# Kernel tuning notes

Hardware: AMD Instinct MI355X
Metric: run time of the kernel (lower is better)

Reference implementation:

```python
import jax, jax.numpy as jnp
import numpy as np

D_MODEL = 1024
N_HEADS = 16
D_K = D_MODEL // N_HEADS
D_FF = 4096
B, S = 2, 2048
EPS = 1e-5


def setup_inputs() -> dict:
    key = jax.random.key(0)
    ks = jax.random.split(key, 16)
    sc = 0.02
    inp = {
        'x': jax.random.normal(ks[0], (B, S, D_MODEL), dtype=jnp.float32),
        'mask': jnp.ones((B, 1, 1, S), dtype=jnp.int32),
        'Wq': jax.random.normal(ks[1], (D_MODEL, D_MODEL), dtype=jnp.float32) * sc,
        'bq': jnp.zeros((D_MODEL,), dtype=jnp.float32),
        'Wk': jax.random.normal(ks[2], (D_MODEL, D_MODEL), dtype=jnp.float32) * sc,
        'bk': jnp.zeros((D_MODEL,), dtype=jnp.float32),
        'Wv': jax.random.normal(ks[3], (D_MODEL, D_MODEL), dtype=jnp.float32) * sc,
        'bv': jnp.zeros((D_MODEL,), dtype=jnp.float32),
        'Wo': jax.random.normal(ks[4], (D_MODEL, D_MODEL), dtype=jnp.float32) * sc,
        'bo': jnp.zeros((D_MODEL,), dtype=jnp.float32),
        'W1': jax.random.normal(ks[5], (D_MODEL, D_FF), dtype=jnp.float32) * sc,
        'b1': jnp.zeros((D_FF,), dtype=jnp.float32),
        'W2': jax.random.normal(ks[6], (D_FF, D_MODEL), dtype=jnp.float32) * sc,
        'b2': jnp.zeros((D_MODEL,), dtype=jnp.float32),
        'g1': jnp.ones((D_MODEL,), dtype=jnp.float32),
        'be1': jnp.zeros((D_MODEL,), dtype=jnp.float32),
        'g2': jnp.ones((D_MODEL,), dtype=jnp.float32),
        'be2': jnp.zeros((D_MODEL,), dtype=jnp.float32),
    }
    return inp


def _layernorm(x, g, b):
    mu = jnp.mean(x, axis=-1, keepdims=True)
    var = jnp.mean(jnp.square(x - mu), axis=-1, keepdims=True)
    return (x - mu) * jax.lax.rsqrt(var + EPS) * g + b


def _split_heads(x):
    b, s, _ = x.shape
    return x.reshape(b, s, N_HEADS, D_K).transpose(0, 2, 1, 3)  # [B,H,S,Dk]


def reference(x, mask, Wq, bq, Wk, bk, Wv, bv, Wo, bo, W1, b1, W2, b2, g1, be1, g2, be2):
    Q = _split_heads(x @ Wq + bq)
    K = _split_heads(x @ Wk + bk)
    V = _split_heads(x @ Wv + bv)
    scores = jnp.einsum('bhqd,bhkd->bhqk', Q, K) / jnp.sqrt(jnp.float32(D_K))
    scores = jnp.where(mask == 0, -jnp.inf, scores)
    attn = jax.nn.softmax(scores, axis=-1)
    ctx = jnp.einsum('bhqk,bhkd->bhqd', attn, V)
    ctx = ctx.transpose(0, 2, 1, 3).reshape(x.shape[0], x.shape[1], D_MODEL)
    attn_out = ctx @ Wo + bo
    h = _layernorm(x + attn_out, g1, be1)
    ff = jax.nn.relu(h @ W1 + b1) @ W2 + b2
    return _layernorm(h + ff, g2, be2)
```

## Files before the change

### kernel.cpp

```cpp
#include <hip/hip_runtime.h>
#include <hip/hip_bf16.h>

#define D_MODELC 1024
#define D_FFC    4096
#define N_HEADSC 16
#define BATCHC   2
#define SEQC     2048
#define M_TOK    (BATCHC*SEQC)

typedef __attribute__((ext_vector_type(4)))  float f32x4;
typedef __attribute__((ext_vector_type(16))) float f32x16;
typedef __attribute__((ext_vector_type(8)))  short s16x8;
using bf16_t = __hip_bfloat16;

static __device__ __forceinline__ unsigned short f2bf_u16(float f) {
  bf16_t h = __float2bfloat16(f);
  return __builtin_bit_cast(unsigned short, h);
}

static __device__ __forceinline__ unsigned int cvt_pk_bf16(float lo, float hi2) {
  unsigned int r;
  asm("v_cvt_pk_bf16_f32 %0, %1, %2" : "=v"(r) : "v"(lo), "v"(hi2));
  return r;
}

#define PSWAP(a, b) asm volatile("v_permlane32_swap_b32 %0, %1" : "+v"(a), "+v"(b))

#define ASYNC_COPY16(dst_lds, src_g) \
  __builtin_amdgcn_global_load_lds((const __attribute__((address_space(1))) void*)(src_g), \
                                   (__attribute__((address_space(3))) void*)(dst_lds), 16, 0, 0)

__global__ __launch_bounds__(256) void k_prep(
    const float* __restrict__ x,
    const float* __restrict__ Wq, const float* __restrict__ Wk,
    const float* __restrict__ Wv, const float* __restrict__ Wo,
    const float* __restrict__ W1, const float* __restrict__ W2,
    const float* __restrict__ bq, const float* __restrict__ bk,
    const float* __restrict__ bv,
    bf16_t* __restrict__ x16, bf16_t* __restrict__ wqkvT, bf16_t* __restrict__ woT,
    bf16_t* __restrict__ w1T, bf16_t* __restrict__ w2T, float* __restrict__ bqkv) {
  __shared__ float tile[32][33];
  const int bidx = blockIdx.x;
  const int tid = threadIdx.x;

  if (bidx < 12288) {
    const float* in;
    bf16_t* out;
    int R, C, bx, by;
    if (bidx < 4096) {
      const int z = bidx >> 10, t = bidx & 1023;
      in = (z == 0) ? Wq : (z == 1) ? Wk : (z == 2) ? Wv : Wo;
      out = (z == 0) ? wqkvT : (z == 1) ? wqkvT + 1024 * 1024
           : (z == 2) ? wqkvT + 2 * 1024 * 1024 : woT;
      R = 1024; C = 1024; bx = t & 31; by = t >> 5;
    } else if (bidx < 8192) {
      const int t = bidx - 4096;
      in = W1; out = w1T; R = 1024; C = 4096; bx = t & 127; by = t >> 7;
    } else {
      const int t = bidx - 8192;
      in = W2; out = w2T; R = 4096; C = 1024; bx = t & 31; by = t >> 5;
    }
    const int tx = tid & 31, ty = tid >> 5;
    const int c0 = bx * 32, r0 = by * 32;
#pragma unroll
    for (int i = 0; i < 4; ++i)
      tile[ty + i * 8][tx] = in[(size_t)(r0 + ty + i * 8) * C + c0 + tx];
    __syncthreads();
#pragma unroll
    for (int i = 0; i < 4; ++i)
      out[(size_t)(c0 + ty + i * 8) * R + r0 + tx] = __float2bfloat16(tile[tx][ty + i * 8]);
  } else if (bidx < 16384) {
    const int i = (bidx - 12288) * 256 + tid;
    float4 v = ((const float4*)x)[i];
    short4 o;
    o.x = (short)f2bf_u16(v.x);
    o.y = (short)f2bf_u16(v.y);
    o.z = (short)f2bf_u16(v.z);
    o.w = (short)f2bf_u16(v.w);
    ((short4*)x16)[i] = o;
  } else {
    const int i = (bidx - 16384) * 256 + tid;
    float v = (i < 1024) ? bq[i] : (i < 2048) ? bk[i - 1024] : bv[i - 2048];
    bqkv[i] = v;
  }
}

#define GBK 64

__global__ __launch_bounds__(256, 2) void k_gemm(
    const bf16_t* __restrict__ A, const bf16_t* __restrict__ BT,
    const float* __restrict__ bias,
    float* __restrict__ p0, float* __restrict__ p1,
    void* __restrict__ Cout, int M, int N, int K,
    int lda, int ldb, int ldc, int mode, int nsplit) {
  __shared__ __align__(16) bf16_t Asm[128 * GBK];
  __shared__ __align__(16) bf16_t Bsm[128 * GBK];

  const int nbn = N / 128;
  const int nwg = gridDim.x;
  const int cpx = nwg >> 3;
  int wg = (blockIdx.x & 7) * cpx + (blockIdx.x >> 3);
  int kslice = 0;
  if (nsplit == 2) { kslice = wg & 1; wg >>= 1; }
  const int mb = wg / nbn, nb = wg % nbn;
  const int row0 = mb * 128, col0 = nb * 128;
  A  += (size_t)kslice * K;
  BT += (size_t)kslice * K;

  const int tid = threadIdx.x;
  const int w = tid >> 6, lane = tid & 63;
  const int lr = lane & 15, lg = lane >> 4;
  const int wr = w >> 1, wc = w & 1;
  const int wbase = tid & 192;

  f32x4 acc[4][4];
#pragma unroll
  for (int m = 0; m < 4; ++m)
#pragma unroll
    for (int n = 0; n < 4; ++n) acc[m][n] = (f32x4){0.f, 0.f, 0.f, 0.f};

  for (int k0 = 0; k0 < K; k0 += GBK) {
    __syncthreads();
#pragma unroll
    for (int i = 0; i < 4; ++i) {
      int c = i * 256 + tid;
      int row = c >> 3;
      int sg = (c & 7) ^ (row & 7);
      ASYNC_COPY16(Asm + (size_t)(i * 256 + wbase) * 8,
                   A + (size_t)(row0 + row) * lda + k0 + sg * 8);
    }
#pragma unroll
    for (int i = 0; i < 4; ++i) {
      int c = i * 256 + tid;
      int row = c >> 3;
      int sg = (c & 7) ^ (row & 7);
      ASYNC_COPY16(Bsm + (size_t)(i * 256 + wbase) * 8,
                   BT + (size_t)(col0 + row) * ldb + k0 + sg * 8);
    }
    __syncthreads();
#pragma unroll
    for (int kst = 0; kst < 2; ++kst) {
      const int sl = ((kst * 4 + lg) ^ (lr & 7)) * 8;
      s16x8 af[4], bfr[4];
#pragma unroll
      for (int m = 0; m < 4; ++m)
        af[m] = *(const s16x8*)(Asm + (size_t)(wr * 64 + m * 16 + lr) * GBK + sl);
#pragma unroll
      for (int n = 0; n < 4; ++n)
        bfr[n] = *(const s16x8*)(Bsm + (size_t)(wc * 64 + n * 16 + lr) * GBK + sl);
#pragma unroll
      for (int m = 0; m < 4; ++m)
#pragma unroll
        for (int n = 0; n < 4; ++n)
          acc[m][n] = __builtin_amdgcn_mfma_f32_16x16x32_bf16(af[m], bfr[n], acc[m][n], 0, 0, 0);
    }
  }

  float* outf = (kslice == 0) ? p0 : p1;
  bf16_t* outh = (bf16_t*)Cout;
#pragma unroll
  for (int m = 0; m < 4; ++m) {
    int grow = row0 + wr * 64 + m * 16 + lg * 4;
#pragma unroll
    for (int n = 0; n < 4; ++n) {
      int gcol = col0 + wc * 64 + n * 16 + lr;
      float bv = (mode == 4) ? 0.f : bias[gcol];
      float cs = (mode == 3 && gcol < 1024) ? 0.18033688f : 1.f;
#pragma unroll
      for (int r = 0; r < 4; ++r) {
        float v = (acc[m][n][r] + bv) * cs;
        size_t idx = (size_t)(grow + r) * ldc + gcol;
        if (mode == 4) {
          outf[idx] = v;
        } else {
          if (mode == 1) v = fmaxf(v, 0.f);
          outh[idx] = __float2bfloat16(v);
        }
      }
    }
  }
}

__global__ __launch_bounds__(256, 4) void k_attn(
    const bf16_t* __restrict__ qkv, const int* __restrict__ mask,
    float* __restrict__ pA, float* __restrict__ pB,
    float* __restrict__ psA, float* __restrict__ psB) {
  const int bid = blockIdx.x;
  const int half = bid >> 9;
  const int inner = bid & 511;
  const int qt = inner & 15;
  const int h  = (inner >> 4) & 15;
  const int b  = inner >> 8;
  const int tid = threadIdx.x;
  const int w = tid >> 6, lane = tid & 63;
  const int l31 = lane & 31, hi = lane >> 5;
  const int wbase = tid & 192;

  __shared__ __align__(16) bf16_t Kl[2][64][64];
  __shared__ __align__(16) bf16_t Vl[2][4096];
  __shared__ __align__(16) float  mskf[2][68];

  const int tokb = b * SEQC;
  const int q0 = qt * 128 + w * 32;
  const int kb0 = half * (SEQC / 2);

  s16x8 qfrag[4];
  {
    const bf16_t* qp = qkv + (size_t)(tokb + q0 + l31) * 3072 + h * 64 + hi * 8;
#pragma unroll
    for (int s = 0; s < 4; ++s) qfrag[s] = *(const s16x8*)(qp + s * 16);
  }

  char* klc = (char*)&Kl[0][0][0];
  bf16_t* Vl0 = &Vl[0][0];
  const unsigned vbase =
      (unsigned)(size_t)(__attribute__((address_space(3))) bf16_t*)Vl0 + lane * 8;

  int vkey0, vd0, vkey1, vd1;
  {
    int c = tid, L = c >> 3;
    int f_ = L >> 4, t_ = (L >> 3) & 1, db_ = (L >> 2) & 1, h_ = (L >> 1) & 1, dl_ = L & 1;
    vkey0 = 16 * f_ + 8 * h_ + 4 * t_ + ((c & 7) >> 1);
    vd0 = ((db_ * 2 + dl_) << 4) + (c & 1) * 8;
  }
  {
    int c = tid + 256, L = c >> 3;
    int f_ = L >> 4, t_ = (L >> 3) & 1, db_ = (L >> 2) & 1, h_ = (L >> 1) & 1, dl_ = L & 1;
    vkey1 = 16 * f_ + 8 * h_ + 4 * t_ + ((c & 7) >> 1);
    vd1 = ((db_ * 2 + dl_) << 4) + (c & 1) * 8;
  }
  const bf16_t* srcV0 = qkv + (size_t)(tokb + kb0 + vkey0) * 3072 + 2048 + (size_t)h * 64 + vd0;
  const bf16_t* srcV1 = qkv + (size_t)(tokb + kb0 + vkey1) * 3072 + 2048 + (size_t)h * 64 + vd1;

  float mreg = 1.f;

#define STAGE_K(buf, kb)                                                              \
  {                                                                                   \
    _Pragma("unroll")                                                                 \
    for (int ii = 0; ii < 2; ++ii) {                                                  \
      int chunk = w * 2 + ii;                                                         \
      int row = chunk * 8 + (lane >> 3);                                              \
      int seg = (lane & 7) ^ (row & 7);                                               \
      const bf16_t* src = qkv + (size_t)(tokb + (kb) + row) * 3072 + 1024 + h * 64 + seg * 8; \
      ASYNC_COPY16(&Kl[buf][chunk * 8][0], src);                                      \
    }                                                                                 \
  }

#define STAGE_V(buf)                                                                  \
  {                                                                                   \
    ASYNC_COPY16(Vl0 + (size_t)(buf) * 4096 + (size_t)wbase * 8, srcV0);              \
    ASYNC_COPY16(Vl0 + (size_t)(buf) * 4096 + (size_t)(256 + wbase) * 8, srcV1);      \
    srcV0 += 64 * 3072;                                                               \
    srcV1 += 64 * 3072;                                                               \
  }

#define STAGE_M(buf, kb)                                                              \
  {                                                                                   \
    if (w == 0) {                                                                     \
      mreg = mask[tokb + (kb) + lane] ? 1.f : 0.f;                                    \
      mskf[buf][lane] = mreg;                                                         \
      unsigned long long z = __ballot(mreg == 0.f);                                   \
      if (lane == 0) mskf[buf][64] = (z == 0ull) ? 1.f : 0.f;                         \
    }                                                                                 \
  }

  STAGE_K(0, kb0)
  STAGE_V(0)
  STAGE_M(0, kb0)

  f32x16 o[2];
#pragma unroll
  for (int d = 0; d < 2; ++d)
#pragma unroll
    for (int i = 0; i < 16; ++i) o[d][i] = 0.f;
  float psum = 0.f;

  __syncthreads();

  for (int kt = 0; kt < SEQC / 128; ++kt) {
    const int kb = kb0 + kt * 64;
    const int cur = kt & 1, nxt = cur ^ 1;
    const bool more = (kt < SEQC / 128 - 1);

    if (more) {
      STAGE_K(nxt, kb + 64)
      STAGE_V(nxt)
      STAGE_M(nxt, kb + 64)
    }

    f32x16 st[2];
#pragma unroll
    for (int kk = 0; kk < 2; ++kk)
#pragma unroll
      for (int i = 0; i < 16; ++i) st[kk][i] = 0.f;
#pragma unroll
    for (int step = 0; step < 4; ++step) {
#pragma unroll
      for (int kb2 = 0; kb2 < 2; ++kb2) {
        int key = kb2 * 32 + l31;
        int seg = (2 * step + hi) ^ (lane & 7);
        s16x8 kf = *(const s16x8*)(klc + cur * 8192 + key * 128 + seg * 16);
        st[kb2] = __builtin_amdgcn_mfma_f32_32x32x16_bf16(kf, qfrag[step], st[kb2], 0, 0, 0);
      }
    }

    const bool allv = (mskf[cur][64] != 0.f);
    s16x8 pf[4];
#pragma unroll
    for (int kb2 = 0; kb2 < 2; ++kb2) {
      float pa[16];
      if (allv) {
#pragma unroll
        for (int i = 0; i < 16; ++i) {
          float e = __builtin_exp2f(st[kb2][i]);
          pa[i] = e;
          psum += e;
        }
      } else {
#pragma unroll
        for (int g = 0; g < 4; ++g) {
          f32x4 mm = *(const f32x4*)((char*)&mskf[cur][0] + (kb2 * 128 + g * 32 + hi * 16));
#pragma unroll
          for (int rr = 0; rr < 4; ++rr) {
            float e = __builtin_exp2f(st[kb2][g * 4 + rr]) * mm[rr];
            pa[g * 4 + rr] = e;
            psum += e;
          }
        }
      }
      unsigned int wv[8];
#pragma unroll
      for (int u = 0; u < 8; ++u) wv[u] = cvt_pk_bf16(pa[2 * u], pa[2 * u + 1]);
      unsigned int a0 = wv[0], b0 = wv[2]; PSWAP(a0, b0);
      unsigned int a1 = wv[1], b1 = wv[3]; PSWAP(a1, b1);
      unsigned int a2 = wv[4], b2 = wv[6]; PSWAP(a2, b2);
      unsigned int a3 = wv[5], b3 = wv[7]; PSWAP(a3, b3);
      uint4 u0 = {a0, a1, b0, b1};
      uint4 u1 = {a2, a3, b2, b3};
      pf[kb2 * 2 + 0] = __builtin_bit_cast(s16x8, u0);
      pf[kb2 * 2 + 1] = __builtin_bit_cast(s16x8, u1);
    }

    const unsigned va = vbase + cur * 8192;
#pragma unroll
    for (int db = 0; db < 2; ++db) {
      ulong tr[4][2];
#pragma unroll
      for (int f = 0; f < 4; ++f)
        asm volatile("ds_read_b64_tr_b16 %0, %2 offset:%c3\n\t"
                     "ds_read_b64_tr_b16 %1, %2 offset:%c4"
                     : "=v"(tr[f][0]), "=v"(tr[f][1])
                     : "v"(va), "i"((f * 16 + db * 4) * 128), "i"((f * 16 + 8 + db * 4) * 128));
      asm volatile("s_waitcnt lgkmcnt(0)" ::: "memory");
      __builtin_amdgcn_sched_barrier(0);
#pragma unroll
      for (int f = 0; f < 4; ++f) {
        ulong2 uv = {tr[f][0], tr[f][1]};
        s16x8 vfr = __builtin_bit_cast(s16x8, uv);
        o[db] = __builtin_amdgcn_mfma_f32_32x32x16_bf16(pf[f], vfr, o[db], 0, 0, 0);
      }
    }

    __syncthreads();
  }

  psum += __shfl_xor(psum, 32);
  float* po = half ? pB : pA;
  float* ps = half ? psB : psA;
#pragma unroll
  for (int dblk = 0; dblk < 2; ++dblk)
#pragma unroll
    for (int r = 0; r < 16; ++r) {
      int qq = (r & 3) + 8 * (r >> 2) + 4 * hi;
      int tok = tokb + q0 + qq;
      po[(size_t)tok * 1024 + h * 64 + dblk * 32 + l31] = o[dblk][r];
    }
  if (hi == 0)
    ps[(size_t)(tokb + q0 + l31) * 16 + h] = psum;
#undef STAGE_K
#undef STAGE_V
#undef STAGE_M
}

__global__ __launch_bounds__(256) void k_attn_merge(
    const float* __restrict__ pA, const float* __restrict__ pB,
    const float* __restrict__ psA, const float* __restrict__ psB,
    bf16_t* __restrict__ ctx) {
  const int row = blockIdx.x, tid = threadIdx.x;
  const size_t base = (size_t)row * 1024;
  const float4 a = ((const float4*)(pA + base))[tid];
  const float4 b = ((const float4*)(pB + base))[tid];
  const int hh = tid >> 4;
  const float rs = psA[row * 16 + hh] + psB[row * 16 + hh];
  const float inv = 1.f / rs;
  short4 ob;
  ob.x = (short)f2bf_u16((a.x + b.x) * inv);
  ob.y = (short)f2bf_u16((a.y + b.y) * inv);
  ob.z = (short)f2bf_u16((a.z + b.z) * inv);
  ob.w = (short)f2bf_u16((a.w + b.w) * inv);
  ((short4*)(ctx + base))[tid] = ob;
}

__global__ __launch_bounds__(256) void k_ln_res2(
    const float* __restrict__ p0, const float* __restrict__ p1,
    const float* __restrict__ res, const float* __restrict__ bias,
    const float* __restrict__ g, const float* __restrict__ be,
    float* __restrict__ outf, bf16_t* __restrict__ outh) {
  const int row = blockIdx.x, tid = threadIdx.x;
  const size_t base = (size_t)row * D_MODELC;
  const float4 a  = ((const float4*)(p0 + base))[tid];
  const float4 bq = ((const float4*)(p1 + base))[tid];
  const float4 c  = ((const float4*)(res + base))[tid];
  const float4 bi = ((const float4*)bias)[tid];
  float4 v;
  v.x = a.x + bq.x + c.x + bi.x;
  v.y = a.y + bq.y + c.y + bi.y;
  v.z = a.z + bq.z + c.z + bi.z;
  v.w = a.w + bq.w + c.w + bi.w;
  float s1 = v.x + v.y + v.z + v.w;
  float s2 = v.x * v.x + v.y * v.y + v.z * v.z + v.w * v.w;
#pragma unroll
  for (int mm = 1; mm < 64; mm <<= 1) {
    s1 += __shfl_xor(s1, mm);
    s2 += __shfl_xor(s2, mm);
  }
  __shared__ float sa[4], sb[4];
  const int wv = tid >> 6;
  if ((tid & 63) == 0) { sa[wv] = s1; sb[wv] = s2; }
  __syncthreads();
  s1 = sa[0] + sa[1] + sa[2] + sa[3];
  s2 = sb[0] + sb[1] + sb[2] + sb[3];
  const float mu = s1 * (1.f / D_MODELC);
  const float var = s2 * (1.f / D_MODELC) - mu * mu;
  const float rsq = rsqrtf(var + 1e-5f);
  const float4 gg = ((const float4*)g)[tid];
  const float4 bb = ((const float4*)be)[tid];
  float4 oo;
  oo.x = (v.x - mu) * rsq * gg.x + bb.x;
  oo.y = (v.y - mu) * rsq * gg.y + bb.y;
  oo.z = (v.z - mu) * rsq * gg.z + bb.z;
  oo.w = (v.w - mu) * rsq * gg.w + bb.w;
  ((float4*)(outf + base))[tid] = oo;
  if (outh) {
    short4 ob;
    ob.x = (short)f2bf_u16(oo.x);
    ob.y = (short)f2bf_u16(oo.y);
    ob.z = (short)f2bf_u16(oo.z);
    ob.w = (short)f2bf_u16(oo.w);
    ((short4*)(outh + base))[tid] = ob;
  }
}

extern "C" void kernel_launch(void* const* d_in, const int* in_sizes, int n_in,
                              void* d_out, int out_size, void* d_ws, size_t ws_size,
                              hipStream_t stream) {
  (void)in_sizes; (void)n_in; (void)out_size; (void)ws_size;
  const float* x   = (const float*)d_in[0];
  const int* mask  = (const int*)d_in[1];
  const float* Wq  = (const float*)d_in[2];
  const float* bq  = (const float*)d_in[3];
  const float* Wk  = (const float*)d_in[4];
  const float* bk  = (const float*)d_in[5];
  const float* Wv  = (const float*)d_in[6];
  const float* bv  = (const float*)d_in[7];
  const float* Wo  = (const float*)d_in[8];
  const float* bo  = (const float*)d_in[9];
  const float* W1  = (const float*)d_in[10];
  const float* b1  = (const float*)d_in[11];
  const float* W2  = (const float*)d_in[12];
  const float* b2  = (const float*)d_in[13];
  const float* g1  = (const float*)d_in[14];
  const float* be1 = (const float*)d_in[15];
  const float* g2  = (const float*)d_in[16];
  const float* be2 = (const float*)d_in[17];

  char* ws = (char*)d_ws;
  const size_t D = D_MODELC, F = D_FFC, M = M_TOK;
  const size_t SZ_X16  = M * D * 2;
  const size_t SZ_QKV  = M * 3 * D * 2;
  bf16_t* x16   = (bf16_t*)ws;
  bf16_t* ff1   = (bf16_t*)ws;
  bf16_t* qkvb  = (bf16_t*)(ws + SZ_X16);
  size_t off = SZ_X16 + SZ_QKV;
  bf16_t* ctx   = (bf16_t*)(ws + off); off += M * D * 2;
  bf16_t* wqkvT = (bf16_t*)(ws + off); off += 3 * D * D * 2;
  bf16_t* woT   = (bf16_t*)(ws + off); off += D * D * 2;
  bf16_t* w1T   = (bf16_t*)(ws + off); off += D * F * 2;
  bf16_t* w2T   = (bf16_t*)(ws + off); off += D * F * 2;
  float*  partA = (float*)(ws + off);  off += M * D * 4;
  float*  hbuf  = (float*)(ws + off);  off += M * D * 4;
  bf16_t* h16   = (bf16_t*)(ws + off); off += M * D * 2;
  float*  partB = (float*)(ws + off);  off += M * D * 4;
  float*  bqkv  = (float*)(ws + off);  off += 3 * D * 4;
  float*  psA   = (float*)(ws + off);  off += M * 16 * 4;
  float*  psB   = (float*)(ws + off);  off += M * 16 * 4;

  k_prep<<<16396, 256, 0, stream>>>(x, Wq, Wk, Wv, Wo, W1, W2, bq, bk, bv,
                                    x16, wqkvT, woT, w1T, w2T, bqkv);

  k_gemm<<<768, 256, 0, stream>>>(x16, wqkvT, bqkv, nullptr, nullptr, qkvb,
                                  4096, 3072, 1024, 1024, 1024, 3072, 3, 1);

  k_attn<<<1024, 256, 0, stream>>>(qkvb, mask, partA, partB, psA, psB);
  k_attn_merge<<<4096, 256, 0, stream>>>(partA, partB, psA, psB, ctx);

  k_gemm<<<512, 256, 0, stream>>>(ctx, woT, nullptr, partA, partB, nullptr,
                                  4096, 1024, 512, 1024, 1024, 1024, 4, 2);
  k_ln_res2<<<4096, 256, 0, stream>>>(partA, partB, x, bo, g1, be1, hbuf, h16);

  k_gemm<<<1024, 256, 0, stream>>>(h16, w1T, b1, nullptr, nullptr, ff1,
                                   4096, 4096, 1024, 1024, 1024, 4096, 1, 1);
  k_gemm<<<512, 256, 0, stream>>>(ff1, w2T, nullptr, partA, partB, nullptr,
                                  4096, 1024, 2048, 4096, 4096, 1024, 4, 2);
  k_ln_res2<<<4096, 256, 0, stream>>>(partA, partB, hbuf, b2, g2, be2, (float*)d_out, nullptr);
}
```

Before: 252.2 us.

## Add 256x256 double-buffered GEMM kernel for QKV and FFN1 projections

Adds a 512-thread GEMM kernel with 256x256 output tiles, two LDS buffers with async copies prefetched two k-steps ahead, split half-K fragment loads, and s_setprio around the MFMA bursts. It replaces the 128x128 kernel for the QKV and FFN up-projections to raise operand reuse per tile and overlap loads with MFMA work. The attention kernel also switches K and mask staging to incrementally advanced pointers, removing per-iteration address math. The larger tile gives fewer workgroups (192 and 256) on a large-CU device, which can leave CUs idle, and uses 128 KB of LDS per block.

```diff
diff --git a/kernel.cpp b/kernel.cpp
--- a/kernel.cpp
+++ b/kernel.cpp
@@ -85,6 +85,120 @@
   }
 }
 
+__global__ __launch_bounds__(512, 2) void k_gemm256(
+    const bf16_t* __restrict__ A, const bf16_t* __restrict__ BT,
+    const float* __restrict__ bias, bf16_t* __restrict__ Cout,
+    int N, int K, int lda, int ldb, int ldc, int mode) {
+  __shared__ __align__(16) bf16_t Ab[2][256][64];
+  __shared__ __align__(16) bf16_t Bb[2][256][64];
+
+  const int nbn = N / 256;
+  const int nwg = gridDim.x;
+  const int cpx = nwg >> 3;
+  const int wg = (blockIdx.x & 7) * cpx + (blockIdx.x >> 3);
+  const int mb = wg / nbn, nb = wg % nbn;
+  const int row0 = mb * 256, col0 = nb * 256;
+
+  const int tid = threadIdx.x;
+  const int w = tid >> 6, lane = tid & 63;
+  const int lr = lane & 15, lg = lane >> 4;
+  const int wr = w >> 2, wc = w & 3;
+  const int s7 = lr & 7;
+
+#define STAGE256(buf, kt_)                                                            \
+  {                                                                                   \
+    const int k0_ = (kt_) * 64;                                                       \
+    _Pragma("unroll")                                                                 \
+    for (int i_ = 0; i_ < 4; ++i_) {                                                  \
+      int c_ = tid + i_ * 512;                                                        \
+      int row_ = c_ >> 3, sg_ = (c_ & 7) ^ (row_ & 7);                                \
+      ASYNC_COPY16(&Ab[buf][0][0] + (size_t)c_ * 8,                                   \
+                   A + (size_t)(row0 + row_) * lda + k0_ + sg_ * 8);                  \
+    }                                                                                 \
+    _Pragma("unroll")                                                                 \
+    for (int i_ = 0; i_ < 4; ++i_) {                                                  \
+      int c_ = tid + i_ * 512;                                                        \
+      int row_ = c_ >> 3, sg_ = (c_ & 7) ^ (row_ & 7);                                \
+      ASYNC_COPY16(&Bb[buf][0][0] + (size_t)c_ * 8,                                   \
+                   BT + (size_t)(col0 + row_) * ldb + k0_ + sg_ * 8);                 \
+    }                                                                                 \
+  }
+
+  f32x4 acc[8][4];
+#pragma unroll
+  for (int m = 0; m < 8; ++m)
+#pragma unroll
+    for (int n = 0; n < 4; ++n) acc[m][n] = (f32x4){0.f, 0.f, 0.f, 0.f};
+
+  const int nt = K / 64;
+  STAGE256(0, 0)
+  STAGE256(1, 1)
+  asm volatile("s_waitcnt vmcnt(8)" ::: "memory");
+  __builtin_amdgcn_sched_barrier(0);
+  __builtin_amdgcn_s_barrier();
+
+  for (int t = 0; t < nt; ++t) {
+    const int cur = t & 1;
+    s16x8 a0[8], b0[4];
+#pragma unroll
+    for (int m = 0; m < 8; ++m)
+      a0[m] = *(const s16x8*)(&Ab[cur][wr * 128 + m * 16 + lr][(lg ^ s7) * 8]);
+#pragma unroll
+    for (int n = 0; n < 4; ++n)
+      b0[n] = *(const s16x8*)(&Bb[cur][wc * 64 + n * 16 + lr][(lg ^ s7) * 8]);
+    __builtin_amdgcn_s_setprio(1);
+#pragma unroll
+    for (int m = 0; m < 8; ++m)
+#pragma unroll
+      for (int n = 0; n < 4; ++n)
+        acc[m][n] = __builtin_amdgcn_mfma_f32_16x16x32_bf16(a0[m], b0[n], acc[m][n], 0, 0, 0);
+    __builtin_amdgcn_s_setprio(0);
+    s16x8 a1[8], b1[4];
+#pragma unroll
+    for (int m = 0; m < 8; ++m)
+      a1[m] = *(const s16x8*)(&Ab[cur][wr * 128 + m * 16 + lr][((4 + lg) ^ s7) * 8]);
+#pragma unroll
+    for (int n = 0; n < 4; ++n)
+      b1[n] = *(const s16x8*)(&Bb[cur][wc * 64 + n * 16 + lr][((4 + lg) ^ s7) * 8]);
+    asm volatile("s_waitcnt lgkmcnt(0)" ::: "memory");
+    __builtin_amdgcn_sched_barrier(0);
+    __builtin_amdgcn_s_barrier();
+    if (t + 2 < nt) STAGE256(cur, t + 2)
+    __builtin_amdgcn_s_setprio(1);
+#pragma unroll
+    for (int m = 0; m < 8; ++m)
+#pragma unroll
+      for (int n = 0; n < 4; ++n)
+        acc[m][n] = __builtin_amdgcn_mfma_f32_16x16x32_bf16(a1[m], b1[n], acc[m][n], 0, 0, 0);
+    __builtin_amdgcn_s_setprio(0);
+    if (t + 2 < nt) {
+      asm volatile("s_waitcnt vmcnt(8)" ::: "memory");
+    } else {
+      asm volatile("s_waitcnt vmcnt(0)" ::: "memory");
+    }
+    __builtin_amdgcn_sched_barrier(0);
+    __builtin_amdgcn_s_barrier();
+  }
+
+#pragma unroll
+  for (int m = 0; m < 8; ++m) {
+    int grow = row0 + wr * 128 + m * 16 + lg * 4;
+#pragma unroll
+    for (int n = 0; n < 4; ++n) {
+      int gcol = col0 + wc * 64 + n * 16 + lr;
+      float bv = bias[gcol];
+      float cs = (mode == 3 && gcol < 1024) ? 0.18033688f : 1.f;
+#pragma unroll
+      for (int r = 0; r < 4; ++r) {
+        float v = (acc[m][n][r] + bv) * cs;
+        if (mode == 1) v = fmaxf(v, 0.f);
+        Cout[(size_t)(grow + r) * ldc + gcol] = __float2bfloat16(v);
+      }
+    }
+  }
+#undef STAGE256
+}
+
 #define GBK 64
 
 __global__ __launch_bounds__(256, 2) void k_gemm(
@@ -165,7 +279,7 @@
     for (int n = 0; n < 4; ++n) {
       int gcol = col0 + wc * 64 + n * 16 + lr;
       float bv = (mode == 4) ? 0.f : bias[gcol];
-      float cs = (mode == 3 && gcol < 1024) ? 0.18033688f : 1.f;
+      float cs = 1.f;
 #pragma unroll
       for (int r = 0; r < 4; ++r) {
         float v = (acc[m][n][r] + bv) * cs;
@@ -231,19 +345,22 @@
   }
   const bf16_t* srcV0 = qkv + (size_t)(tokb + kb0 + vkey0) * 3072 + 2048 + (size_t)h * 64 + vd0;
   const bf16_t* srcV1 = qkv + (size_t)(tokb + kb0 + vkey1) * 3072 + 2048 + (size_t)h * 64 + vd1;
+  const int krow0 = ((w * 2 + 0) * 8) + (lane >> 3);
+  const int krow1 = ((w * 2 + 1) * 8) + (lane >> 3);
+  const bf16_t* srcK0 = qkv + (size_t)(tokb + kb0 + krow0) * 3072 + 1024 + (size_t)h * 64
+                        + (((lane & 7) ^ (krow0 & 7)) * 8);
+  const bf16_t* srcK1 = qkv + (size_t)(tokb + kb0 + krow1) * 3072 + 1024 + (size_t)h * 64
+                        + (((lane & 7) ^ (krow1 & 7)) * 8);
+  const int* mptr = mask + tokb + kb0 + lane;
 
   float mreg = 1.f;
 
-#define STAGE_K(buf, kb)                                                              \
+#define STAGE_K(buf)                                                                  \
   {                                                                                   \
-    _Pragma("unroll")                                                                 \
-    for (int ii = 0; ii < 2; ++ii) {                                                  \
-      int chunk = w * 2 + ii;                                                         \
-      int row = chunk * 8 + (lane >> 3);                                              \
-      int seg = (lane & 7) ^ (row & 7);                                               \
-      const bf16_t* src = qkv + (size_t)(tokb + (kb) + row) * 3072 + 1024 + h * 64 + seg * 8; \
-      ASYNC_COPY16(&Kl[buf][chunk * 8][0], src);                                      \
-    }                                                                                 \
+    ASYNC_COPY16(&Kl[buf][(w * 2 + 0) * 8][0], srcK0);                                \
+    ASYNC_COPY16(&Kl[buf][(w * 2 + 1) * 8][0], srcK1);                                \
+    srcK0 += 64 * 3072;                                                               \
+    srcK1 += 64 * 3072;                                                               \
   }
 
 #define STAGE_V(buf)                                                                  \
@@ -254,19 +371,20 @@
     srcV1 += 64 * 3072;                                                               \
   }
 
-#define STAGE_M(buf, kb)                                                              \
+#define STAGE_M(buf)                                                                  \
   {                                                                                   \
     if (w == 0) {                                                                     \
-      mreg = mask[tokb + (kb) + lane] ? 1.f : 0.f;                                    \
+      mreg = *mptr ? 1.f : 0.f;                                                       \
       mskf[buf][lane] = mreg;                                                         \
       unsigned long long z = __ballot(mreg == 0.f);                                   \
       if (lane == 0) mskf[buf][64] = (z == 0ull) ? 1.f : 0.f;                         \
     }                                                                                 \
-  }
-
-  STAGE_K(0, kb0)
+    mptr += 64;                                                                       \
+  }
+
+  STAGE_K(0)
   STAGE_V(0)
-  STAGE_M(0, kb0)
+  STAGE_M(0)
 
   f32x16 o[2];
 #pragma unroll
@@ -278,14 +396,13 @@
   __syncthreads();
 
   for (int kt = 0; kt < SEQC / 128; ++kt) {
-    const int kb = kb0 + kt * 64;
     const int cur = kt & 1, nxt = cur ^ 1;
     const bool more = (kt < SEQC / 128 - 1);
 
     if (more) {
-      STAGE_K(nxt, kb + 64)
+      STAGE_K(nxt)
       STAGE_V(nxt)
-      STAGE_M(nxt, kb + 64)
+      STAGE_M(nxt)
     }
 
     f32x16 st[2];
@@ -498,8 +615,8 @@
   k_prep<<<16396, 256, 0, stream>>>(x, Wq, Wk, Wv, Wo, W1, W2, bq, bk, bv,
                                     x16, wqkvT, woT, w1T, w2T, bqkv);
 
-  k_gemm<<<768, 256, 0, stream>>>(x16, wqkvT, bqkv, nullptr, nullptr, qkvb,
-                                  4096, 3072, 1024, 1024, 1024, 3072, 3, 1);
+  k_gemm256<<<192, 512, 0, stream>>>(x16, wqkvT, bqkv, qkvb,
+                                     3072, 1024, 1024, 1024, 3072, 3);
 
   k_attn<<<1024, 256, 0, stream>>>(qkvb, mask, partA, partB, psA, psB);
   k_attn_merge<<<4096, 256, 0, stream>>>(partA, partB, psA, psB, ctx);
@@ -508,8 +625,8 @@
                                   4096, 1024, 512, 1024, 1024, 1024, 4, 2);
   k_ln_res2<<<4096, 256, 0, stream>>>(partA, partB, x, bo, g1, be1, hbuf, h16);
 
-  k_gemm<<<1024, 256, 0, stream>>>(h16, w1T, b1, nullptr, nullptr, ff1,
-                                   4096, 4096, 1024, 1024, 1024, 4096, 1, 1);
+  k_gemm256<<<256, 512, 0, stream>>>(h16, w1T, b1, ff1,
+                                     4096, 1024, 1024, 1024, 4096, 1);
   k_gemm<<<512, 256, 0, stream>>>(ff1, w2T, nullptr, partA, partB, nullptr,
                                   4096, 1024, 2048, 4096, 4096, 1024, 4, 2);
   k_ln_res2<<<4096, 256, 0, stream>>>(partA, partB, hbuf, b2, g2, be2, (float*)d_out, nullptr);
```

Result: faster. 234.1 us (-7.1%).
